# Performance work log

Hardware: AMD Instinct MI355X
Metric: run time of the kernel (lower is better)

Reference implementation:

```python
import jax, jax.numpy as jnp
import numpy as np

B, C, H, W = 4, 128, 128, 128
CO = 128           # output channels of deformable conv
KH = KW = 3
K = KH * KW        # 9 kernel taps


def setup_inputs() -> dict:
    key = jax.random.key(0)
    k1, k2, k3, k4 = jax.random.split(key, 4)
    x = jax.random.normal(k1, (B, C, H, W), jnp.float32)
    # conv_offset: Conv2D(3*K channels, 3x3, stride 1, same, bias), channels_first
    offset_w = jax.random.normal(k2, (3 * K, C, KH, KW), jnp.float32) * 0.01
    offset_b = jnp.zeros((3 * K,), jnp.float32)
    # deformable conv weights: [CO, C, KH, KW] + bias
    deform_w = jax.random.normal(k3, (CO, C, KH, KW), jnp.float32) * (1.0 / np.sqrt(C * K))
    deform_b = jax.random.normal(k4, (CO,), jnp.float32) * 0.01
    return {"x": x, "offset_w": offset_w, "offset_b": offset_b,
            "deform_w": deform_w, "deform_b": deform_b}


def _bilinear_gather(x, y, xc):
    """Bilinear sample x [B,C,H,W] at float coords y, xc [B,K,H,W].
    Out-of-bounds samples contribute zero. Returns [B,C,K,H,W]."""
    Bn, Cn, Hn, Wn = x.shape
    y0 = jnp.floor(y)
    x0 = jnp.floor(xc)
    wy = y - y0   # frac weights
    wx = xc - x0
    xf = x.reshape(Bn, Cn, Hn * Wn)

    def corner(yc, xcc, wgt):
        valid = (yc >= 0) & (yc < Hn) & (xcc >= 0) & (xcc < Wn)
        yi = jnp.clip(yc, 0, Hn - 1).astype(jnp.int32)
        xi = jnp.clip(xcc, 0, Wn - 1).astype(jnp.int32)
        idx = (yi * Wn + xi).reshape(Bn, 1, -1)            # [B,1,K*H*W]
        g = jnp.take_along_axis(xf, idx, axis=2)           # [B,C,K*H*W]
        g = g.reshape(Bn, Cn, *yc.shape[1:])               # [B,C,K,H,W]
        return g * (wgt * valid)[:, None]

    return (corner(y0,     x0,     (1 - wy) * (1 - wx))
          + corner(y0,     x0 + 1, (1 - wy) * wx)
          + corner(y0 + 1, x0,     wy * (1 - wx))
          + corner(y0 + 1, x0 + 1, wy * wx))


def reference(x, offset_w, offset_b, deform_w, deform_b):
    # offset/mask predicting conv (stride 1, SAME, channels_first)
    wi = jax.lax.conv_general_dilated(
        x, offset_w, window_strides=(1, 1), padding='SAME',
        dimension_numbers=('NCHW', 'OIHW', 'NCHW')) + offset_b[None, :, None, None]
    o1, o2, m = jnp.split(wi, 3, axis=1)      # each [B,K,H,W]
    dy, dx = o1, o2                            # offset = concat(o1, o2)
    mask = jax.nn.sigmoid(m)

    # kernel tap displacements relative to center (SAME padding, 3x3)
    ky = jnp.repeat(jnp.arange(KH), KW) - (KH // 2)   # [K]
    kx = jnp.tile(jnp.arange(KW), KH) - (KW // 2)     # [K]
    y = dy + jnp.arange(H, dtype=jnp.float32)[None, None, :, None] + ky[None, :, None, None]
    xs = dx + jnp.arange(W, dtype=jnp.float32)[None, None, None, :] + kx[None, :, None, None]

    samp = _bilinear_gather(x, y, xs)          # [B,C,K,H,W]
    # modulated accumulation: sum over ci and kernel taps
    out = jnp.einsum('bckhw,ock->bohw', samp * mask[:, None], deform_w.reshape(CO, C, K))
    return out + deform_b[None, :, None, None]
```

## Files before the change

kernel.cpp:

```cpp
#include <hip/hip_runtime.h>
#include <hip/hip_bf16.h>
#include <math.h>

#define Bn 4
#define Cn 128
#define Hn 128
#define Wn 128
#define COn 128
#define HWn (Hn*Wn)
#define NPIX (Bn*HWn)

typedef __attribute__((ext_vector_type(8))) short bf16x8;
typedef __attribute__((ext_vector_type(4))) float f32x4;

__device__ inline unsigned short f2bf_hw(float f) {
    __hip_bfloat16 h = __float2bfloat16(f);
    return *reinterpret_cast<unsigned short*>(&h);
}
__device__ inline unsigned pack_bf2(float lo, float hi) {
    __hip_bfloat162 h2;
    h2.x = __float2bfloat16(lo);
    h2.y = __float2bfloat16(hi);
    return *reinterpret_cast<unsigned*>(&h2);
}
__device__ inline float bflo(unsigned w) {
    union { unsigned u; float f; } cv; cv.u = w << 16; return cv.f;
}
__device__ inline float bfhi(unsigned w) {
    union { unsigned u; float f; } cv; cv.u = w & 0xffff0000u; return cv.f;
}
__device__ inline void async_copy16(const void* g, void* l) {
    __builtin_amdgcn_global_load_lds(
        (const __attribute__((address_space(1))) unsigned int*)g,
        (__attribute__((address_space(3))) unsigned int*)l, 16, 0, 0);
}

__global__ __launch_bounds__(256) void k_prep(
    const float* __restrict__ x, unsigned short* __restrict__ xt,
    const float* __restrict__ dw, short* __restrict__ pw,
    const float* __restrict__ ow, short* __restrict__ pwo)
{
    __shared__ unsigned short t[Wn][Cn + 2];
    const int tid = threadIdx.x;
    const int bid = blockIdx.x;

    if (bid < 512) {
        const int bh = bid;
        const int b  = bh >> 7, h = bh & 127;
        const float* xp = x + (((size_t)b*Cn) << 14) + h*Wn;
        for (int i = tid; i < Cn*Wn; i += 256) {
            int c = i >> 7, w = i & 127;
            t[w][c] = f2bf_hw(xp[(size_t)c*HWn + w]);
        }
        __syncthreads();
        unsigned* xto = (unsigned*)(xt + ((size_t)bh << 7) * Cn);
        for (int j = tid; j < Wn*(Cn/2); j += 256) {
            int w = j >> 6, cp = j & 63;
            xto[(size_t)w*64 + cp] = *(const unsigned*)&t[w][2*cp];
        }
    } else if (bid < 584) {
        const int blk = (bid - 512)*4 + (tid >> 6);
        const int ks  = blk >> 3;
        const int ot  = blk & 7;
        const int cchunk = ks / 9;
        const int tap    = ks - cchunk*9;
        const int l   = tid & 63;
        const int oc  = ot*16 + (l & 15);
        const int kk0 = (l >> 4)*8;
        bf16x8 fr;
        #pragma unroll
        for (int j = 0; j < 8; ++j) {
            int c = cchunk*32 + kk0 + j;
            fr[j] = (short)f2bf_hw(dw[oc*1152 + c*9 + tap]);
        }
        *(bf16x8*)(pw + ((size_t)blk*64 + l)*8) = fr;
    } else {
        const int blk = (bid - 584)*4 + (tid >> 6);
        const int ks  = blk >> 1;
        const int ot  = blk & 1;
        const int cchunk = ks / 9;
        const int tap    = ks - cchunk*9;
        const int l   = tid & 63;
        const int oc  = ot*16 + (l & 15);
        const int kk0 = (l >> 4)*8;
        bf16x8 fr;
        #pragma unroll
        for (int j = 0; j < 8; ++j) {
            int c = cchunk*32 + kk0 + j;
            fr[j] = (oc < 27) ? (short)f2bf_hw(ow[oc*1152 + c*9 + tap]) : (short)0;
        }
        *(bf16x8*)(pwo + ((size_t)blk*64 + l)*8) = fr;
    }
}

__global__ __launch_bounds__(256) void k_deform_fused(
    const unsigned short* __restrict__ xt, const char* __restrict__ pw,
    const short* __restrict__ pwo, const float* __restrict__ ob,
    const float* __restrict__ db, float* __restrict__ out)
{
    __shared__ __align__(16) char a_lds[2][8192];
    __shared__ uint4 lmeta[64][9];
    const int tid = threadIdx.x;
    const int wid = tid >> 6;
    const int l   = tid & 63;
    const int lm  = l & 15;
    const int lg  = l >> 4;
    const int bid = blockIdx.x;
    const int wg  = (bid & 7)*128 + (bid >> 3);
    const int p0  = wg*64;
    const int p   = p0 + wid*16 + lm;
    const int b   = p >> 14;
    const int hw  = p & (HWn - 1);
    const int h   = hw >> 7;
    const int w   = hw & (Wn - 1);

    {
        f32x4 oacc[2];
        oacc[0] = (f32x4){0.f,0.f,0.f,0.f};
        oacc[1] = (f32x4){0.f,0.f,0.f,0.f};
        const int4* apg = (const int4*)pwo;

        #pragma unroll 1
        for (int ks = 0; ks < 36; ++ks) {
            const int cchunk = ks / 9;
            const int tap    = ks - cchunk*9;
            const int y  = h + tap/3 - 1;
            const int xx = w + (tap - (tap/3)*3) - 1;
            const bool ok = (y >= 0) & (y < Hn) & (xx >= 0) & (xx < Wn);
            const int yc  = min(max(y, 0), Hn-1);
            const int xc  = min(max(xx, 0), Wn-1);
            int4 v = *(const int4*)(xt + (((size_t)(b*Hn + yc)*Wn + xc) << 7)
                                       + cchunk*32 + lg*8);
            if (!ok) v = make_int4(0,0,0,0);
            const int4* ap = apg + (size_t)(ks*2)*64 + l;
            oacc[0] = __builtin_amdgcn_mfma_f32_16x16x32_bf16(
                __builtin_bit_cast(bf16x8, ap[0]),  __builtin_bit_cast(bf16x8, v), oacc[0], 0, 0, 0);
            oacc[1] = __builtin_amdgcn_mfma_f32_16x16x32_bf16(
                __builtin_bit_cast(bf16x8, ap[64]), __builtin_bit_cast(bf16x8, v), oacc[1], 0, 0, 0);
        }

        float* ol = (float*)a_lds;
        #pragma unroll
        for (int ot = 0; ot < 2; ++ot)
            #pragma unroll
            for (int r = 0; r < 4; ++r) {
                int oc = ot*16 + lg*4 + r;
                ol[(wid*16 + lm)*33 + oc] = oacc[ot][r] + ((oc < 27) ? ob[oc] : 0.0f);
            }

        const int pbase = p0 + wid*16;
        for (int i = l; i < 144; i += 64) {
            const int tap = i >> 4;
            const int px  = i & 15;
            const int pp  = pbase + px;
            const int bb  = pp >> 14;
            const int hh  = (pp & (HWn-1)) >> 7;
            const int ww  = pp & 127;
            float dy = ol[(wid*16 + px)*33 + tap];
            float dx = ol[(wid*16 + px)*33 + 9 + tap];
            float mr = ol[(wid*16 + px)*33 + 18 + tap];
            float m  = 1.0f / (1.0f + __expf(-mr));
            float yf = (float)(hh + tap/3 - 1) + dy;
            float xf = (float)(ww + (tap - (tap/3)*3) - 1) + dx;
            float y0f = floorf(yf), x0f = floorf(xf);
            int   y0  = (int)y0f,  x0  = (int)x0f;
            float wy = yf - y0f, wx = xf - x0f;
            int yi0 = min(max(y0,     0), Hn-1), yi1 = min(max(y0 + 1, 0), Hn-1);
            int xi0 = min(max(x0,     0), Wn-1), xi1 = min(max(x0 + 1, 0), Wn-1);
            float vy0 = ((y0 >= 0)     & (y0 < Hn))     ? 1.0f : 0.0f;
            float vy1 = ((y0 + 1 >= 0) & (y0 + 1 < Hn)) ? 1.0f : 0.0f;
            float vx0 = ((x0 >= 0)     & (x0 < Wn))     ? 1.0f : 0.0f;
            float vx1 = ((x0 + 1 >= 0) & (x0 + 1 < Wn)) ? 1.0f : 0.0f;
            float w0_ = m * (1.0f-wy) * (1.0f-wx) * vy0 * vx0;
            float w1_ = m * (1.0f-wy) * wx        * vy0 * vx1;
            float w2_ = m * wy        * (1.0f-wx) * vy1 * vx0;
            float w3_ = m * wy        * wx        * vy1 * vx1;
            uint4 mq;
            mq.x = (unsigned)(((bb << 14) + yi0*Wn + xi0) << 8);
            mq.y = (unsigned)((xi1 - xi0)*256) | (unsigned)((yi1 - yi0)*32768);
            mq.z = pack_bf2(w0_, w1_);
            mq.w = pack_bf2(w2_, w3_);
            lmeta[wid*16 + px][tap] = mq;
        }
    }
    __syncthreads();

    f32x4 acc[8];
    #pragma unroll
    for (int ot = 0; ot < 8; ++ot) acc[ot] = (f32x4){0.f,0.f,0.f,0.f};

    const char* xb = (const char*)xt;
    const int   ml = wid*16 + lm;

    #define STAGE(ks_, buf_) {                                                  \
        const char* g0 = pw + (size_t)(ks_)*8192 + wid*1024 + l*16;             \
        async_copy16(g0,        (void*)&a_lds[buf_][wid*1024]);                 \
        async_copy16(g0 + 4096, (void*)&a_lds[buf_][4096 + wid*1024]);          \
    }

    STAGE(0, 0);
    int cur = 0;

    #pragma unroll 1
    for (int ks = 0; ks < 36; ++ks) {
        const int cchunk = ks / 9;
        const int tap    = ks - cchunk*9;
        __syncthreads();
        if (ks + 1 < 36) STAGE(ks + 1, cur ^ 1);

        const uint4 mq = lmeta[ml][tap];
        const unsigned offc = mq.x + (unsigned)(cchunk*64 + lg*16);
        const unsigned dxb  = mq.y & 256u;
        const unsigned dyb  = mq.y & 32768u;

        const uint4 q0 = *(const uint4*)(xb + offc);
        const uint4 q1 = *(const uint4*)(xb + (offc + dxb));
        const uint4 q2 = *(const uint4*)(xb + (offc + dyb));
        const uint4 q3 = *(const uint4*)(xb + (offc + dyb + dxb));

        const float w0_ = bflo(mq.z), w1_ = bfhi(mq.z);
        const float w2_ = bflo(mq.w), w3_ = bfhi(mq.w);

        unsigned bw[4];
        const unsigned* u0 = (const unsigned*)&q0;
        const unsigned* u1 = (const unsigned*)&q1;
        const unsigned* u2 = (const unsigned*)&q2;
        const unsigned* u3 = (const unsigned*)&q3;
        #pragma unroll
        for (int q = 0; q < 4; ++q) {
            float lo = w0_*bflo(u0[q]) + w1_*bflo(u1[q]) + w2_*bflo(u2[q]) + w3_*bflo(u3[q]);
            float hi = w0_*bfhi(u0[q]) + w1_*bfhi(u1[q]) + w2_*bfhi(u2[q]) + w3_*bfhi(u3[q]);
            bw[q] = pack_bf2(lo, hi);
        }
        int4 bi = make_int4(bw[0], bw[1], bw[2], bw[3]);
        bf16x8 bfrag = __builtin_bit_cast(bf16x8, bi);

        #pragma unroll
        for (int ot = 0; ot < 8; ++ot) {
            int4 av = *(const int4*)&a_lds[cur][(ot*64 + l)*16];
            acc[ot] = __builtin_amdgcn_mfma_f32_16x16x32_bf16(
                __builtin_bit_cast(bf16x8, av), bfrag, acc[ot], 0, 0, 0);
        }
        cur ^= 1;
    }
    #undef STAGE

    #pragma unroll
    for (int ot = 0; ot < 8; ++ot) {
        #pragma unroll
        for (int r = 0; r < 4; ++r) {
            int oc = ot*16 + lg*4 + r;
            out[((size_t)(b*COn + oc) << 14) + hw] = acc[ot][r] + db[oc];
        }
    }
}

extern "C" void kernel_launch(void* const* d_in, const int* in_sizes, int n_in,
                              void* d_out, int out_size, void* d_ws, size_t ws_size,
                              hipStream_t stream) {
    const float* x  = (const float*)d_in[0];
    const float* ow = (const float*)d_in[1];
    const float* ob = (const float*)d_in[2];
    const float* dw = (const float*)d_in[3];
    const float* db = (const float*)d_in[4];
    float* out  = (float*)d_out;

    short*          pw  = (short*)d_ws;
    short*          pwo = (short*)((char*)d_ws + 294912);
    unsigned short* xtp = (unsigned short*)((char*)d_ws + 368640);

    hipLaunchKernelGGL(k_prep, dim3(602), dim3(256), 0, stream,
                       x, xtp, dw, pw, ow, pwo);
    hipLaunchKernelGGL(k_deform_fused, dim3(NPIX/64), dim3(256), 0, stream,
                       xtp, (const char*)pw, pwo, ob, db, out);
}
```

Baseline: 112.9 us.

## Software-pipeline bilinear gathers one step ahead with manual waitcnt control

Restructures the 36-step K loop into a two-stage software pipeline. The four bilinear corner loads for step k+1 are issued before the step-k interpolation and MFMA work, using double-buffered register sets and explicit vmcnt waits and sched barriers. The goal is to hide global gather latency behind compute. It costs extra VGPRs, which may reduce occupancy. It also swaps __syncthreads for a raw s_barrier with hand-tuned waitcnts, which relies on correct counting of the async LDS copies.

```diff
diff --git a/kernel.cpp b/kernel.cpp
--- a/kernel.cpp
+++ b/kernel.cpp
@@ -191,6 +191,7 @@
 
     const char* xb = (const char*)xt;
     const int   ml = wid*16 + lm;
+    int cur = 0;
 
     #define STAGE(ks_, buf_) {                                                  \
         const char* g0 = pw + (size_t)(ks_)*8192 + wid*1024 + l*16;             \
@@ -198,51 +199,79 @@
         async_copy16(g0 + 4096, (void*)&a_lds[buf_][4096 + wid*1024]);          \
     }
 
+    #define PREFETCH(KS1, MQO, Q0, Q1, Q2, Q3) {                                \
+        const int cc1_ = (KS1)/9;                                               \
+        const int tp1_ = (KS1) - cc1_*9;                                        \
+        MQO = lmeta[ml][tp1_];                                                  \
+        const unsigned of_ = MQO.x + (unsigned)(cc1_*64 + lg*16);               \
+        const unsigned dx_ = MQO.y & 256u;                                      \
+        const unsigned dy_ = MQO.y & 32768u;                                    \
+        Q0 = *(const uint4*)(xb + of_);                                         \
+        Q1 = *(const uint4*)(xb + (of_ + dx_));                                 \
+        Q2 = *(const uint4*)(xb + (of_ + dy_));                                 \
+        Q3 = *(const uint4*)(xb + (of_ + dy_ + dx_));                           \
+    }
+
+    #define COMPUTE(MQI, Q0, Q1, Q2, Q3) {                                      \
+        const float w0_ = bflo(MQI.z), w1_ = bfhi(MQI.z);                       \
+        const float w2_ = bflo(MQI.w), w3_ = bfhi(MQI.w);                       \
+        unsigned bw[4];                                                         \
+        const unsigned* u0 = (const unsigned*)&Q0;                              \
+        const unsigned* u1 = (const unsigned*)&Q1;                              \
+        const unsigned* u2 = (const unsigned*)&Q2;                              \
+        const unsigned* u3 = (const unsigned*)&Q3;                              \
+        _Pragma("unroll")                                                       \
+        for (int q = 0; q < 4; ++q) {                                           \
+            float lo = w0_*bflo(u0[q]) + w1_*bflo(u1[q]) + w2_*bflo(u2[q]) + w3_*bflo(u3[q]); \
+            float hi = w0_*bfhi(u0[q]) + w1_*bfhi(u1[q]) + w2_*bfhi(u2[q]) + w3_*bfhi(u3[q]); \
+            bw[q] = pack_bf2(lo, hi);                                           \
+        }                                                                       \
+        int4 bi = make_int4(bw[0], bw[1], bw[2], bw[3]);                        \
+        bf16x8 bfrag = __builtin_bit_cast(bf16x8, bi);                          \
+        _Pragma("unroll")                                                       \
+        for (int ot = 0; ot < 8; ++ot) {                                        \
+            int4 av = *(const int4*)&a_lds[cur][(ot*64 + l)*16];                \
+            acc[ot] = __builtin_amdgcn_mfma_f32_16x16x32_bf16(                  \
+                __builtin_bit_cast(bf16x8, av), bfrag, acc[ot], 0, 0, 0);       \
+        }                                                                       \
+    }
+
+    #define PBODY(KS, MQI, I0, I1, I2, I3, MQO, O0, O1, O2, O3) {               \
+        __builtin_amdgcn_s_barrier();                                           \
+        STAGE((KS)+1, cur ^ 1);                                                 \
+        __builtin_amdgcn_sched_barrier(0);                                      \
+        PREFETCH((KS)+1, MQO, O0, O1, O2, O3);                                  \
+        asm volatile("s_waitcnt vmcnt(6)" ::: "memory");                        \
+        __builtin_amdgcn_sched_barrier(0);                                      \
+        COMPUTE(MQI, I0, I1, I2, I3);                                           \
+        asm volatile("s_waitcnt vmcnt(4)" ::: "memory");                        \
+        cur ^= 1;                                                               \
+    }
+
+    uint4 mqA, a0, a1, a2, a3;
+    uint4 mqB, b0, b1, b2, b3;
+
     STAGE(0, 0);
-    int cur = 0;
+    __builtin_amdgcn_sched_barrier(0);
+    PREFETCH(0, mqA, a0, a1, a2, a3);
+    asm volatile("s_waitcnt vmcnt(4)" ::: "memory");
 
     #pragma unroll 1
-    for (int ks = 0; ks < 36; ++ks) {
-        const int cchunk = ks / 9;
-        const int tap    = ks - cchunk*9;
-        __syncthreads();
-        if (ks + 1 < 36) STAGE(ks + 1, cur ^ 1);
-
-        const uint4 mq = lmeta[ml][tap];
-        const unsigned offc = mq.x + (unsigned)(cchunk*64 + lg*16);
-        const unsigned dxb  = mq.y & 256u;
-        const unsigned dyb  = mq.y & 32768u;
-
-        const uint4 q0 = *(const uint4*)(xb + offc);
-        const uint4 q1 = *(const uint4*)(xb + (offc + dxb));
-        const uint4 q2 = *(const uint4*)(xb + (offc + dyb));
-        const uint4 q3 = *(const uint4*)(xb + (offc + dyb + dxb));
-
-        const float w0_ = bflo(mq.z), w1_ = bfhi(mq.z);
-        const float w2_ = bflo(mq.w), w3_ = bfhi(mq.w);
-
-        unsigned bw[4];
-        const unsigned* u0 = (const unsigned*)&q0;
-        const unsigned* u1 = (const unsigned*)&q1;
-        const unsigned* u2 = (const unsigned*)&q2;
-        const unsigned* u3 = (const unsigned*)&q3;
-        #pragma unroll
-        for (int q = 0; q < 4; ++q) {
-            float lo = w0_*bflo(u0[q]) + w1_*bflo(u1[q]) + w2_*bflo(u2[q]) + w3_*bflo(u3[q]);
-            float hi = w0_*bfhi(u0[q]) + w1_*bfhi(u1[q]) + w2_*bfhi(u2[q]) + w3_*bfhi(u3[q]);
-            bw[q] = pack_bf2(lo, hi);
-        }
-        int4 bi = make_int4(bw[0], bw[1], bw[2], bw[3]);
-        bf16x8 bfrag = __builtin_bit_cast(bf16x8, bi);
-
-        #pragma unroll
-        for (int ot = 0; ot < 8; ++ot) {
-            int4 av = *(const int4*)&a_lds[cur][(ot*64 + l)*16];
-            acc[ot] = __builtin_amdgcn_mfma_f32_16x16x32_bf16(
-                __builtin_bit_cast(bf16x8, av), bfrag, acc[ot], 0, 0, 0);
-        }
-        cur ^= 1;
-    }
+    for (int k2 = 0; k2 < 17; ++k2) {
+        const int ks = k2*2;
+        PBODY(ks,     mqA, a0, a1, a2, a3, mqB, b0, b1, b2, b3);
+        PBODY(ks + 1, mqB, b0, b1, b2, b3, mqA, a0, a1, a2, a3);
+    }
+    PBODY(34, mqA, a0, a1, a2, a3, mqB, b0, b1, b2, b3);
+    {
+        __builtin_amdgcn_s_barrier();
+        asm volatile("s_waitcnt vmcnt(0)" ::: "memory");
+        __builtin_amdgcn_sched_barrier(0);
+        COMPUTE(mqB, b0, b1, b2, b3);
+    }
+    #undef PBODY
+    #undef COMPUTE
+    #undef PREFETCH
     #undef STAGE
 
     #pragma unroll
```

Measured after the change: 113.4 us. No clear change (+0.4%).
